# Performance work log

Measured on AMD Instinct MI355X. Metric: run time of the kernel, lower is better.

Reference implementation:

```python
import jax, jax.numpy as jnp
import numpy as np

H = 1024  # hidden_size
S = 2048  # src_max_len
B = 32    # batch


def setup_inputs() -> dict:
    key = jax.random.key(0)
    k1, k2, k3, k4 = jax.random.split(key, 4)
    scale_w = 1.0 / np.sqrt(2 * H)  # torch Linear default-ish init scale
    scale_v = 1.0 / np.sqrt(H)
    return {
        "decoder_hidden": jax.random.normal(k1, (1, B, H), dtype=jnp.float32),
        "encoder_outputs": jax.random.normal(k2, (S, B, H), dtype=jnp.float32),
        # w: Linear(2H -> H, no bias). Split into decoder half Wd and encoder half We
        # so the [B,S,2H] concat never needs to be materialized (same math).
        "Wd": jax.random.uniform(k3, (H, H), dtype=jnp.float32, minval=-scale_w, maxval=scale_w),
        "We": jax.random.uniform(jax.random.fold_in(k3, 1), (H, H), dtype=jnp.float32, minval=-scale_w, maxval=scale_w),
        # v: Linear(H -> 1, no bias)
        "v": jax.random.uniform(k4, (H,), dtype=jnp.float32, minval=-scale_v, maxval=scale_v),
    }


def reference(decoder_hidden, encoder_outputs, Wd, We, v):
    # decoder_hidden: [1, B, H] -> [B, 1, H]; encoder_outputs: [S, B, H] -> [B, S, H]
    dec = jnp.transpose(decoder_hidden, (1, 0, 2))   # [B, 1, H]
    enc = jnp.transpose(encoder_outputs, (1, 0, 2))  # [B, S, H]
    # tanh(W_a [h_t; h_s]) == tanh(dec @ Wd^T-part + enc @ We^T-part); here Wd/We
    # are stored as [H_in, H_out] so plain matmul applies.
    energy = jnp.tanh(dec @ Wd + enc @ We)           # [B, S, H] (dec broadcasts over S)
    logits = jnp.einsum("bsh,h->bs", energy, v)       # [B, S]
    attn_scores = jax.nn.softmax(logits, axis=1)[..., None]  # [B, S, 1]
    attn_values = jnp.sum(enc * attn_scores, axis=1)  # [B, H]
    return attn_values, attn_scores
```

## Files before the change

kernel.cpp:

```cpp
#include <hip/hip_runtime.h>

#define H 1024
#define S 2048
#define B 32
#define M (S*B)
#define NSC 16

typedef short bf16x8 __attribute__((ext_vector_type(8)));
typedef float f32x4 __attribute__((ext_vector_type(4)));

__device__ __forceinline__ unsigned short f2bf(float f) {
    unsigned int u = __builtin_bit_cast(unsigned int, f);
    u += 0x7FFFu + ((u >> 16) & 1u);
    return (unsigned short)(u >> 16);
}

__device__ __forceinline__ float tanh_fast(float x) {
    float e = __expf(2.f * x);
    return 1.f - 2.f / (e + 1.f);
}

__device__ __forceinline__ void gload_lds16(const void* g, void* l) {
    __builtin_amdgcn_global_load_lds((const __attribute__((address_space(1))) void*)g,
                                     (__attribute__((address_space(3))) void*)l, 16, 0, 0);
}

__global__ __launch_bounds__(256) void convert_enc(const float* __restrict__ enc,
                                                   unsigned short* __restrict__ encBF) {
    const size_t total = (size_t)M * H / 8;
    for (size_t idx = (size_t)blockIdx.x * 256 + threadIdx.x; idx < total;
         idx += (size_t)gridDim.x * 256) {
        const float4* p = (const float4*)(enc + idx * 8);
        float4 x = p[0], y = p[1];
        bf16x8 c;
        c[0] = (short)f2bf(x.x); c[1] = (short)f2bf(x.y);
        c[2] = (short)f2bf(x.z); c[3] = (short)f2bf(x.w);
        c[4] = (short)f2bf(y.x); c[5] = (short)f2bf(y.y);
        c[6] = (short)f2bf(y.z); c[7] = (short)f2bf(y.w);
        *(bf16x8*)(encBF + idx * 8) = c;
    }
}

__global__ __launch_bounds__(256) void transpose_we(const float* __restrict__ We,
                                                    unsigned short* __restrict__ WeT) {
    __shared__ float t[64][65];
    int tx = threadIdx.x & 63, ty = threadIdx.x >> 6;
    int n0 = blockIdx.x * 64, k0 = blockIdx.y * 64;
#pragma unroll
    for (int q = 0; q < 16; ++q) {
        int kk = ty * 16 + q;
        t[kk][tx] = We[(size_t)(k0 + kk) * H + n0 + tx];
    }
    __syncthreads();
#pragma unroll
    for (int q = 0; q < 16; ++q) {
        int nn = ty * 16 + q;
        WeT[(size_t)(n0 + nn) * H + k0 + tx] = f2bf(t[tx][nn]);
    }
}

__global__ __launch_bounds__(256) void dec_proj(const float* __restrict__ dec,
                                                const float* __restrict__ Wd,
                                                float* __restrict__ dvec) {
    __shared__ float ds[H];
    int b = blockIdx.y, jc = blockIdx.x, t = threadIdx.x;
    for (int i = t; i < H; i += 256) ds[i] = dec[b * H + i];
    __syncthreads();
    int j = jc * 256 + t;
    float acc = 0.f;
#pragma unroll 8
    for (int h = 0; h < H; ++h) acc += ds[h] * Wd[(size_t)h * H + j];
    dvec[b * H + j] = acc;
}

__global__ __launch_bounds__(256) void gemm_logits2(const unsigned short* __restrict__ encBF,
                                                    const unsigned short* __restrict__ WeT,
                                                    const float* __restrict__ dvec,
                                                    const float* __restrict__ v,
                                                    float* __restrict__ part) {
    __shared__ unsigned short As[128 * 64];
    __shared__ unsigned short Bs[128 * 64];
    int tid = threadIdx.x, bid = blockIdx.x;
    int swz = (bid & 7) * 512 + (bid >> 3);
    int bm = swz >> 3, bn = swz & 7;
    int lane = tid & 63, wid = tid >> 6;
    int wm = wid >> 1, wn = wid & 1;

    f32x4 acc[4][4] = {};

    int rsub = lane >> 3;
    int gslot = (lane & 7) ^ rsub;
    const unsigned short* aP[4];
    const unsigned short* bP[4];
    unsigned short* aL[4];
    unsigned short* bL[4];
#pragma unroll
    for (int q = 0; q < 4; ++q) {
        int c = wid * 4 + q;
        int grow = c * 8 + rsub;
        aP[q] = encBF + (size_t)(bm * 128 + grow) * H + gslot * 8;
        bP[q] = WeT + (size_t)(bn * 128 + grow) * H + gslot * 8;
        aL[q] = &As[c * 512];
        bL[q] = &Bs[c * 512];
    }

    for (int kt = 0; kt < 16; ++kt) {
        if (kt) __syncthreads();
#pragma unroll
        for (int q = 0; q < 4; ++q) gload_lds16(aP[q] + kt * 64, aL[q]);
#pragma unroll
        for (int q = 0; q < 4; ++q) gload_lds16(bP[q] + kt * 64, bL[q]);
        __syncthreads();
#pragma unroll
        for (int kh = 0; kh < 2; ++kh) {
            bf16x8 a[4], bfr[4];
#pragma unroll
            for (int m = 0; m < 4; ++m) {
                int row = wm * 64 + m * 16 + (lane & 15);
                int slot = (kh * 4 + (lane >> 4)) ^ (row & 7);
                a[m] = *(const bf16x8*)&As[row * 64 + slot * 8];
            }
#pragma unroll
            for (int n = 0; n < 4; ++n) {
                int row = wn * 64 + n * 16 + (lane & 15);
                int slot = (kh * 4 + (lane >> 4)) ^ (row & 7);
                bfr[n] = *(const bf16x8*)&Bs[row * 64 + slot * 8];
            }
#pragma unroll
            for (int m = 0; m < 4; ++m)
#pragma unroll
                for (int n = 0; n < 4; ++n)
                    acc[m][n] = __builtin_amdgcn_mfma_f32_16x16x32_bf16(a[m], bfr[n], acc[m][n], 0, 0, 0);
        }
    }

    float vj[4];
#pragma unroll
    for (int n = 0; n < 4; ++n) vj[n] = v[bn * 128 + wn * 64 + n * 16 + (lane & 15)];
    float pv[4][4];
#pragma unroll
    for (int m = 0; m < 4; ++m) {
#pragma unroll
        for (int i = 0; i < 4; ++i) {
            int rg = bm * 128 + wm * 64 + m * 16 + (lane >> 4) * 4 + i;
            int bb = rg & (B - 1);
            float p = 0.f;
#pragma unroll
            for (int n = 0; n < 4; ++n) {
                int j = bn * 128 + wn * 64 + n * 16 + (lane & 15);
                p += vj[n] * tanh_fast(dvec[bb * H + j] + acc[m][n][i]);
            }
            p += __shfl_xor(p, 1);
            p += __shfl_xor(p, 2);
            p += __shfl_xor(p, 4);
            p += __shfl_xor(p, 8);
            pv[m][i] = p;
        }
    }
    __syncthreads();
    float* red = (float*)As;
    if (wn == 1) {
#pragma unroll
        for (int m = 0; m < 4; ++m)
#pragma unroll
            for (int i = 0; i < 4; ++i) {
                int rl = wm * 64 + m * 16 + (lane >> 4) * 4 + i;
                if ((lane & 15) == 0) red[rl] = pv[m][i];
            }
    }
    __syncthreads();
    if (wn == 0) {
#pragma unroll
        for (int m = 0; m < 4; ++m)
#pragma unroll
            for (int i = 0; i < 4; ++i) {
                int rl = wm * 64 + m * 16 + (lane >> 4) * 4 + i;
                int rg = bm * 128 + rl;
                if ((lane & 15) == 0) part[(size_t)rg * 8 + bn] = pv[m][i] + red[rl];
            }
    }
}

__global__ __launch_bounds__(256) void softmax_k(const float* __restrict__ part,
                                                 float* __restrict__ scores) {
    int b = blockIdx.x, tid = threadIdx.x;
    int lane = tid & 63, wid = tid >> 6;
    __shared__ float red[4];
    __shared__ float red2[4];
    float lg[8];
    float mx = -1e30f;
#pragma unroll
    for (int q = 0; q < 8; ++q) {
        int s = q * 256 + tid;
        const float4* pr = (const float4*)(part + ((size_t)(s * B + b)) * 8);
        float4 x = pr[0], y = pr[1];
        float L = ((x.x + x.y) + (x.z + x.w)) + ((y.x + y.y) + (y.z + y.w));
        lg[q] = L;
        mx = fmaxf(mx, L);
    }
#pragma unroll
    for (int off = 32; off; off >>= 1) mx = fmaxf(mx, __shfl_xor(mx, off));
    if (lane == 0) red[wid] = mx;
    __syncthreads();
    mx = fmaxf(fmaxf(red[0], red[1]), fmaxf(red[2], red[3]));
    float sum = 0.f;
#pragma unroll
    for (int q = 0; q < 8; ++q) {
        lg[q] = expf(lg[q] - mx);
        sum += lg[q];
    }
#pragma unroll
    for (int off = 32; off; off >>= 1) sum += __shfl_xor(sum, off);
    if (lane == 0) red2[wid] = sum;
    __syncthreads();
    sum = (red2[0] + red2[1]) + (red2[2] + red2[3]);
    float inv = 1.f / sum;
#pragma unroll
    for (int q = 0; q < 8; ++q) scores[b * S + q * 256 + tid] = lg[q] * inv;
}

__global__ __launch_bounds__(256) void weighted_sum(const float* __restrict__ enc,
                                                    const float* __restrict__ scores,
                                                    float* __restrict__ part2) {
    __shared__ float sl[128];
    int t = threadIdx.x;
    int hx = blockIdx.x, b = blockIdx.y, sc = blockIdx.z;
    if (t < 128) sl[t] = scores[b * S + sc * 128 + t];
    __syncthreads();
    int h = hx * 256 + t;
    const float* ep = enc + ((size_t)(sc * 128) * B) * H + (size_t)b * H + h;
    float acc = 0.f;
#pragma unroll 4
    for (int s = 0; s < 128; ++s) acc += ep[(size_t)s * B * H] * sl[s];
    part2[((size_t)sc * B + b) * H + h] = acc;
}

__global__ __launch_bounds__(256) void reduce_vals(const float* __restrict__ part2,
                                                   float* __restrict__ out) {
    int i = blockIdx.x * 256 + threadIdx.x;
    float a = 0.f;
#pragma unroll
    for (int c = 0; c < NSC; ++c) a += part2[(size_t)c * B * H + i];
    out[i] = a;
}

extern "C" void kernel_launch(void* const* d_in, const int* in_sizes, int n_in,
                              void* d_out, int out_size, void* d_ws, size_t ws_size,
                              hipStream_t stream) {
    const float* dec = (const float*)d_in[0];
    const float* enc = (const float*)d_in[1];
    const float* Wd  = (const float*)d_in[2];
    const float* We  = (const float*)d_in[3];
    const float* v   = (const float*)d_in[4];
    float* out = (float*)d_out;

    char* ws = (char*)d_ws;
    unsigned short* WeT = (unsigned short*)ws;
    float* dvec  = (float*)(ws + (2u << 20));
    float* part  = (float*)(ws + (3u << 20));
    float* part2 = (float*)(ws + (5u << 20));
    unsigned short* encBF = (unsigned short*)(ws + ((size_t)8 << 20));

    transpose_we<<<dim3(16, 16), 256, 0, stream>>>(We, WeT);
    dec_proj<<<dim3(4, B), 256, 0, stream>>>(dec, Wd, dvec);
    convert_enc<<<4096, 256, 0, stream>>>(enc, encBF);
    gemm_logits2<<<4096, 256, 0, stream>>>(encBF, WeT, dvec, v, part);
    softmax_k<<<B, 256, 0, stream>>>(part, out + B * H);
    weighted_sum<<<dim3(4, B, NSC), 256, 0, stream>>>(enc, out + B * H, part2);
    reduce_vals<<<128, 256, 0, stream>>>(part2, out);
}
```

Before: 367.9 us.

## Fuse prep kernels into one launch, widen softmax, vectorize weighted sum

The three prep kernels (enc bf16 conversion, We transpose, decoder projection) become a single launch that picks its role from the block index, saving launch overhead and letting the small jobs overlap the large conversion. Softmax now uses 1024 threads per batch row. The weighted sum uses float4 loads with 64-row chunks (NSC=32), and the final reduction is vectorized to match. part and part2 now share workspace memory, which is safe only because softmax finishes reading part before weighted_sum writes part2.

```diff
diff --git a/kernel.cpp b/kernel.cpp
--- a/kernel.cpp
+++ b/kernel.cpp
@@ -4,7 +4,7 @@
 #define S 2048
 #define B 32
 #define M (S*B)
-#define NSC 16
+#define NSC 32
 
 typedef short bf16x8 __attribute__((ext_vector_type(8)));
 typedef float f32x4 __attribute__((ext_vector_type(4)));
@@ -25,52 +25,53 @@
                                      (__attribute__((address_space(3))) void*)l, 16, 0, 0);
 }
 
-__global__ __launch_bounds__(256) void convert_enc(const float* __restrict__ enc,
-                                                   unsigned short* __restrict__ encBF) {
-    const size_t total = (size_t)M * H / 8;
-    for (size_t idx = (size_t)blockIdx.x * 256 + threadIdx.x; idx < total;
-         idx += (size_t)gridDim.x * 256) {
-        const float4* p = (const float4*)(enc + idx * 8);
-        float4 x = p[0], y = p[1];
-        bf16x8 c;
-        c[0] = (short)f2bf(x.x); c[1] = (short)f2bf(x.y);
-        c[2] = (short)f2bf(x.z); c[3] = (short)f2bf(x.w);
-        c[4] = (short)f2bf(y.x); c[5] = (short)f2bf(y.y);
-        c[6] = (short)f2bf(y.z); c[7] = (short)f2bf(y.w);
-        *(bf16x8*)(encBF + idx * 8) = c;
-    }
-}
-
-__global__ __launch_bounds__(256) void transpose_we(const float* __restrict__ We,
-                                                    unsigned short* __restrict__ WeT) {
-    __shared__ float t[64][65];
-    int tx = threadIdx.x & 63, ty = threadIdx.x >> 6;
-    int n0 = blockIdx.x * 64, k0 = blockIdx.y * 64;
-#pragma unroll
-    for (int q = 0; q < 16; ++q) {
-        int kk = ty * 16 + q;
-        t[kk][tx] = We[(size_t)(k0 + kk) * H + n0 + tx];
-    }
-    __syncthreads();
-#pragma unroll
-    for (int q = 0; q < 16; ++q) {
-        int nn = ty * 16 + q;
-        WeT[(size_t)(n0 + nn) * H + k0 + tx] = f2bf(t[tx][nn]);
-    }
-}
-
-__global__ __launch_bounds__(256) void dec_proj(const float* __restrict__ dec,
-                                                const float* __restrict__ Wd,
-                                                float* __restrict__ dvec) {
-    __shared__ float ds[H];
-    int b = blockIdx.y, jc = blockIdx.x, t = threadIdx.x;
-    for (int i = t; i < H; i += 256) ds[i] = dec[b * H + i];
-    __syncthreads();
-    int j = jc * 256 + t;
-    float acc = 0.f;
+__global__ __launch_bounds__(256) void prep(const float* __restrict__ enc,
+                                            unsigned short* __restrict__ encBF,
+                                            const float* __restrict__ We,
+                                            unsigned short* __restrict__ WeT,
+                                            const float* __restrict__ dec,
+                                            const float* __restrict__ Wd,
+                                            float* __restrict__ dvec) {
+    __shared__ float shbuf[64 * 65];
+    int bid = blockIdx.x, t = threadIdx.x;
+    if (bid < 4096) {
+        const size_t total = (size_t)M * H / 8;
+        for (size_t idx = (size_t)bid * 256 + t; idx < total; idx += (size_t)4096 * 256) {
+            const float4* p = (const float4*)(enc + idx * 8);
+            float4 x = p[0], y = p[1];
+            bf16x8 c;
+            c[0] = (short)f2bf(x.x); c[1] = (short)f2bf(x.y);
+            c[2] = (short)f2bf(x.z); c[3] = (short)f2bf(x.w);
+            c[4] = (short)f2bf(y.x); c[5] = (short)f2bf(y.y);
+            c[6] = (short)f2bf(y.z); c[7] = (short)f2bf(y.w);
+            *(bf16x8*)(encBF + idx * 8) = c;
+        }
+    } else if (bid < 4352) {
+        int b2 = bid - 4096;
+        int tx = t & 63, ty = t >> 6;
+        int n0 = (b2 & 15) * 64, k0 = (b2 >> 4) * 64;
+#pragma unroll
+        for (int q = 0; q < 16; ++q) {
+            int kk = ty * 16 + q;
+            shbuf[kk * 65 + tx] = We[(size_t)(k0 + kk) * H + n0 + tx];
+        }
+        __syncthreads();
+#pragma unroll
+        for (int q = 0; q < 16; ++q) {
+            int nn = ty * 16 + q;
+            WeT[(size_t)(n0 + nn) * H + k0 + tx] = f2bf(shbuf[tx * 65 + nn]);
+        }
+    } else {
+        int b3 = bid - 4352;
+        int jc = b3 & 3, b = b3 >> 2;
+        for (int i = t; i < H; i += 256) shbuf[i] = dec[b * H + i];
+        __syncthreads();
+        int j = jc * 256 + t;
+        float acc = 0.f;
 #pragma unroll 8
-    for (int h = 0; h < H; ++h) acc += ds[h] * Wd[(size_t)h * H + j];
-    dvec[b * H + j] = acc;
+        for (int h = 0; h < H; ++h) acc += shbuf[h] * Wd[(size_t)h * H + j];
+        dvec[b * H + j] = acc;
+    }
 }
 
 __global__ __launch_bounds__(256) void gemm_logits2(const unsigned short* __restrict__ encBF,
@@ -181,17 +182,17 @@
     }
 }
 
-__global__ __launch_bounds__(256) void softmax_k(const float* __restrict__ part,
-                                                 float* __restrict__ scores) {
+__global__ __launch_bounds__(1024) void softmax_k(const float* __restrict__ part,
+                                                  float* __restrict__ scores) {
     int b = blockIdx.x, tid = threadIdx.x;
     int lane = tid & 63, wid = tid >> 6;
-    __shared__ float red[4];
-    __shared__ float red2[4];
-    float lg[8];
+    __shared__ float red[16];
+    __shared__ float red2[16];
+    float lg[2];
     float mx = -1e30f;
 #pragma unroll
-    for (int q = 0; q < 8; ++q) {
-        int s = q * 256 + tid;
+    for (int q = 0; q < 2; ++q) {
+        int s = q * 1024 + tid;
         const float4* pr = (const float4*)(part + ((size_t)(s * B + b)) * 8);
         float4 x = pr[0], y = pr[1];
         float L = ((x.x + x.y) + (x.z + x.w)) + ((y.x + y.y) + (y.z + y.w));
@@ -202,10 +203,12 @@
     for (int off = 32; off; off >>= 1) mx = fmaxf(mx, __shfl_xor(mx, off));
     if (lane == 0) red[wid] = mx;
     __syncthreads();
-    mx = fmaxf(fmaxf(red[0], red[1]), fmaxf(red[2], red[3]));
+    mx = red[0];
+#pragma unroll
+    for (int w = 1; w < 16; ++w) mx = fmaxf(mx, red[w]);
     float sum = 0.f;
 #pragma unroll
-    for (int q = 0; q < 8; ++q) {
+    for (int q = 0; q < 2; ++q) {
         lg[q] = expf(lg[q] - mx);
         sum += lg[q];
     }
@@ -213,35 +216,43 @@
     for (int off = 32; off; off >>= 1) sum += __shfl_xor(sum, off);
     if (lane == 0) red2[wid] = sum;
     __syncthreads();
-    sum = (red2[0] + red2[1]) + (red2[2] + red2[3]);
+    sum = 0.f;
+#pragma unroll
+    for (int w = 0; w < 16; ++w) sum += red2[w];
     float inv = 1.f / sum;
 #pragma unroll
-    for (int q = 0; q < 8; ++q) scores[b * S + q * 256 + tid] = lg[q] * inv;
+    for (int q = 0; q < 2; ++q) scores[b * S + q * 1024 + tid] = lg[q] * inv;
 }
 
 __global__ __launch_bounds__(256) void weighted_sum(const float* __restrict__ enc,
                                                     const float* __restrict__ scores,
                                                     float* __restrict__ part2) {
-    __shared__ float sl[128];
-    int t = threadIdx.x;
-    int hx = blockIdx.x, b = blockIdx.y, sc = blockIdx.z;
-    if (t < 128) sl[t] = scores[b * S + sc * 128 + t];
-    __syncthreads();
-    int h = hx * 256 + t;
-    const float* ep = enc + ((size_t)(sc * 128) * B) * H + (size_t)b * H + h;
-    float acc = 0.f;
+    __shared__ float sl[64];
+    int t = threadIdx.x, b = blockIdx.x, sc = blockIdx.y;
+    if (t < 64) sl[t] = scores[b * S + sc * 64 + t];
+    __syncthreads();
+    const float4* ep = (const float4*)(enc + ((size_t)(sc * 64) * B + b) * H) + t;
+    float4 a = {0.f, 0.f, 0.f, 0.f};
 #pragma unroll 4
-    for (int s = 0; s < 128; ++s) acc += ep[(size_t)s * B * H] * sl[s];
-    part2[((size_t)sc * B + b) * H + h] = acc;
+    for (int s = 0; s < 64; ++s) {
+        float4 e = ep[(size_t)s * B * H / 4];
+        float w = sl[s];
+        a.x += e.x * w; a.y += e.y * w; a.z += e.z * w; a.w += e.w * w;
+    }
+    ((float4*)(part2 + ((size_t)sc * B + b) * H))[t] = a;
 }
 
 __global__ __launch_bounds__(256) void reduce_vals(const float* __restrict__ part2,
                                                    float* __restrict__ out) {
-    int i = blockIdx.x * 256 + threadIdx.x;
-    float a = 0.f;
-#pragma unroll
-    for (int c = 0; c < NSC; ++c) a += part2[(size_t)c * B * H + i];
-    out[i] = a;
+    int i4 = blockIdx.x * 256 + threadIdx.x;
+    const float4* p4 = (const float4*)part2;
+    float4 a = {0.f, 0.f, 0.f, 0.f};
+#pragma unroll
+    for (int c = 0; c < NSC; ++c) {
+        float4 e = p4[(size_t)c * (B * H / 4) + i4];
+        a.x += e.x; a.y += e.y; a.z += e.z; a.w += e.w;
+    }
+    ((float4*)out)[i4] = a;
 }
 
 extern "C" void kernel_launch(void* const* d_in, const int* in_sizes, int n_in,
@@ -255,17 +266,15 @@
     float* out = (float*)d_out;
 
     char* ws = (char*)d_ws;
-    unsigned short* WeT = (unsigned short*)ws;
-    float* dvec  = (float*)(ws + (2u << 20));
-    float* part  = (float*)(ws + (3u << 20));
-    float* part2 = (float*)(ws + (5u << 20));
+    float* part  = (float*)ws;
+    float* part2 = (float*)ws;
+    unsigned short* WeT = (unsigned short*)(ws + (4u << 20));
+    float* dvec  = (float*)(ws + (6u << 20));
     unsigned short* encBF = (unsigned short*)(ws + ((size_t)8 << 20));
 
-    transpose_we<<<dim3(16, 16), 256, 0, stream>>>(We, WeT);
-    dec_proj<<<dim3(4, B), 256, 0, stream>>>(dec, Wd, dvec);
-    convert_enc<<<4096, 256, 0, stream>>>(enc, encBF);
+    prep<<<4480, 256, 0, stream>>>(enc, encBF, We, WeT, dec, Wd, dvec);
     gemm_logits2<<<4096, 256, 0, stream>>>(encBF, WeT, dvec, v, part);
-    softmax_k<<<B, 256, 0, stream>>>(part, out + B * H);
-    weighted_sum<<<dim3(4, B, NSC), 256, 0, stream>>>(enc, out + B * H, part2);
-    reduce_vals<<<128, 256, 0, stream>>>(part2, out);
-}
+    softmax_k<<<B, 1024, 0, stream>>>(part, out + B * H);
+    weighted_sum<<<dim3(B, NSC), 256, 0, stream>>>(enc, out + B * H, part2);
+    reduce_vals<<<32, 256, 0, stream>>>(part2, out);
+}
```

After: 354.4 us. 1.04x faster.
